# Kernel tuning notes

Measured on AMD Instinct MI355X. Metric: run time of the kernel, lower is better.

The kernel has to match this reference:

```python
import jax, jax.numpy as jnp
import numpy as np

DEG = [1, 72, 201, 816, 1790, 3756, 6923, 12768, 20286, 31710, 51623, 82296, 124280, 177576, 251115, 326064, 395760, 456840, 506179, 516200, 507003, 493746, 489256, 453936, 420025, 411320, 427761, 420700, 420500, 426780, 414284, 407008, 394053, 360910, 322245, 313704, 282902, 270940, 237783, 209000, 193766, 177870, 162110, 144848, 121230, 112700, 93483, 88512, 72275, 80700, 68799, 56784, 42665, 30996, 25630, 12936, 9804, 8584, 5251, 3480, 3111, 2728, 1890, 1472, 1235, 330, 201, 68, 69, 0, 71]
_d = np.array(DEG, dtype=np.float64)
AVG_LOG = float((np.log(np.arange(len(_d)) + 1.0) * _d).sum() / _d.sum())  # avg_deg['log']

N_NODES, N_EDGES, N_GRAPHS = 10000, 100000, 64
TOWERS, F, F_OUT, N_LAYERS = 5, 75, 15, 4


def setup_inputs() -> dict:
    key = jax.random.key(0)
    ks = jax.random.split(key, 32)
    r = lambda i, shape: jax.random.normal(ks[i], shape, jnp.float32) * 0.1
    return {
        "x": jax.random.normal(ks[0], (N_NODES, 14), jnp.float32),
        "edge_index": jax.random.randint(ks[1], (2, N_EDGES), 0, N_NODES, dtype=jnp.int32),
        "edge_attr": jax.random.normal(ks[2], (N_EDGES, 4), jnp.float32),
        "batch": jnp.sort(jax.random.randint(ks[3], (N_NODES,), 0, N_GRAPHS, dtype=jnp.int32)),
        "node_emb_w": r(4, (14, F)), "node_emb_b": r(5, (F,)),
        "edge_emb_w": r(6, (4, 50)), "edge_emb_b": r(7, (50,)),
        "ee_w": r(8, (N_LAYERS, 50, F)), "ee_b": r(9, (N_LAYERS, F)),
        "pre_w": r(10, (N_LAYERS, TOWERS, 3 * F, F)), "pre_b": r(11, (N_LAYERS, TOWERS, F)),
        "post_w": r(12, (N_LAYERS, TOWERS, 13 * F, F_OUT)), "post_b": r(13, (N_LAYERS, TOWERS, F_OUT)),
        "lin_w": r(14, (N_LAYERS, F, F)), "lin_b": r(15, (N_LAYERS, F)),
        "bn_g": jnp.ones((N_LAYERS, F), jnp.float32), "bn_b": jnp.zeros((N_LAYERS, F), jnp.float32),
        "mlp_w1": r(16, (F, 50)), "mlp_b1": r(17, (50,)),
        "mlp_w2": r(18, (50, 25)), "mlp_b2": r(19, (25,)),
        "mlp_w3": r(20, (25, 1)), "mlp_b3": r(21, (1,)),
    }


def _pna_conv(x, src, dst, ea, ee_w, ee_b, pre_w, pre_b, post_w, post_b, lin_w, lin_b):
    # x: [N, F]; ea: [E, edge_dim]; divide_input=False so every tower sees full F.
    N = x.shape[0]
    e = ea @ ee_w + ee_b                                   # edge_encoder  [E, F]
    h = jnp.concatenate([x[dst], x[src], e], axis=-1)       # [x_i, x_j, e] [E, 3F]
    m = jnp.einsum('ef,tfg->etg', h, pre_w) + pre_b         # per-tower pre nn [E, T, F]
    cnt = jax.ops.segment_sum(jnp.ones((m.shape[0],), x.dtype), dst, N)  # in-degree [N]
    cnt1 = jnp.maximum(cnt, 1.0)[:, None, None]
    mean = jax.ops.segment_sum(m, dst, N) / cnt1
    mean_sq = jax.ops.segment_sum(m * m, dst, N) / cnt1
    std = jnp.sqrt(jax.nn.relu(mean_sq - mean * mean) + 1e-5)
    has = (cnt > 0)[:, None, None]
    mn = jnp.where(has, jax.ops.segment_min(m, dst, N), 0.0)
    mx = jnp.where(has, jax.ops.segment_max(m, dst, N), 0.0)
    agg = jnp.concatenate([mean, mn, mx, std], axis=-1)     # [N, T, 4F]
    scl = jnp.log(cnt1 + 1.0) / AVG_LOG                     # amplification scaler
    out = jnp.concatenate([agg, agg * scl, agg / scl], -1)  # identity/amp/atten [N, T, 12F]
    x_rep = jnp.broadcast_to(x[:, None, :], (N, TOWERS, x.shape[1]))
    out = jnp.concatenate([x_rep, out], axis=-1)            # [N, T, 13F]
    out = jnp.einsum('ntf,tfg->ntg', out, post_w) + post_b  # per-tower post nn [N, T, F_out]
    return out.reshape(N, -1) @ lin_w + lin_b               # [N, F]


def _bn(x, g, b):
    mu = x.mean(0)
    var = x.var(0)  # biased, as torch BatchNorm1d uses for normalization
    return (x - mu) * jax.lax.rsqrt(var + 1e-5) * g + b


def reference(x, edge_index, edge_attr, batch, node_emb_w, node_emb_b, edge_emb_w, edge_emb_b,
              ee_w, ee_b, pre_w, pre_b, post_w, post_b, lin_w, lin_b, bn_g, bn_b,
              mlp_w1, mlp_b1, mlp_w2, mlp_b2, mlp_w3, mlp_b3):
    src, dst = edge_index[0], edge_index[1]
    h = x @ node_emb_w + node_emb_b
    ea = edge_attr @ edge_emb_w + edge_emb_b
    for i in range(N_LAYERS):
        h = jax.nn.relu(_bn(_pna_conv(h, src, dst, ea, ee_w[i], ee_b[i], pre_w[i], pre_b[i],
                                      post_w[i], post_b[i], lin_w[i], lin_b[i]), bn_g[i], bn_b[i]))
    per_atom = h
    g = jax.ops.segment_sum(h, batch, N_GRAPHS)             # global_add_pool [G, F]
    g = jax.nn.relu(g @ mlp_w1 + mlp_b1)
    g = jax.nn.relu(g @ mlp_w2 + mlp_b2)
    g = (g @ mlp_w3 + mlp_b3).reshape(-1)                   # num_out==1 -> view(-1)
    return (g, per_atom)
```

## Files before the change

### kernel.cpp

```cpp
#include <hip/hip_runtime.h>
#include <math.h>

#define NN 10000
#define NE 100000
#define NGR 64
#define NT 5
#define FD 75
#define FOUT 15
#define NLAY 4
#define MAXB 1792

typedef __bf16 bf16;
typedef __bf16 bf16x8 __attribute__((ext_vector_type(8)));
typedef float f32x4 __attribute__((ext_vector_type(4)));

__device__ inline unsigned pk2(float a, float b) {
  bf16 x = (bf16)a, y = (bf16)b;
  unsigned short ux, uy;
  __builtin_memcpy(&ux, &x, 2); __builtin_memcpy(&uy, &y, 2);
  return (unsigned)ux | ((unsigned)uy << 16);
}


__global__ __launch_bounds__(256) void k_node_emb(const float* __restrict__ x,
    const float* __restrict__ w, const float* __restrict__ b, bf16* __restrict__ hbf) {
  int idx = blockIdx.x * 256 + threadIdx.x;
  if (idx >= NN * FD) return;
  int n = idx / FD, f = idx - n * FD;
  float acc = b[f];
#pragma unroll
  for (int k = 0; k < 14; ++k) acc += x[n * 14 + k] * w[k * FD + f];
  hbf[n * 80 + f] = (bf16)acc;
}

__global__ __launch_bounds__(256) void k_hpad(bf16* __restrict__ hbf) {
  int idx = blockIdx.x * 256 + threadIdx.x;
  if (idx >= NN * 5) return;
  int n = idx / 5, f = 75 + idx % 5;
  hbf[n * 80 + f] = (bf16)0.f;
}

__global__ __launch_bounds__(256) void k_edge4(const float* __restrict__ eattr,
    bf16* __restrict__ eabf4) {
  int idx = blockIdx.x * 256 + threadIdx.x;
  if (idx >= NE * 8) return;
  int e = idx >> 3, c = idx & 7;
  eabf4[idx] = (c < 4) ? (bf16)eattr[e * 4 + c] : (bf16)0.f;
}

__global__ __launch_bounds__(256) void k_count(const int* __restrict__ dst, int* __restrict__ deg) {
  int e = blockIdx.x * 256 + threadIdx.x;
  if (e < NE) atomicAdd(&deg[dst[e]], 1);
}

__global__ __launch_bounds__(1024) void k_scan(const int* __restrict__ deg, int* __restrict__ rowptr) {
  __shared__ int buf[1024];
  __shared__ int carry;
  int tid = threadIdx.x;
  if (tid == 0) carry = 0;
  __syncthreads();
  for (int base = 0; base < NN; base += 1024) {
    int i = base + tid;
    int v = (i < NN) ? deg[i] : 0;
    buf[tid] = v;
    __syncthreads();
    for (int off = 1; off < 1024; off <<= 1) {
      int t = (tid >= off) ? buf[tid - off] : 0;
      __syncthreads();
      buf[tid] += t;
      __syncthreads();
    }
    int inc = buf[tid];
    int tot = buf[1023];
    if (i < NN) rowptr[i + 1] = carry + inc;
    __syncthreads();
    if (tid == 0) carry += tot;
    __syncthreads();
  }
  if (tid == 0) rowptr[0] = 0;
}

__global__ __launch_bounds__(256) void k_scl(const int* __restrict__ deg, float* __restrict__ scl,
                                             float* __restrict__ iscl, float inv_avg_log) {
  int n = blockIdx.x * 256 + threadIdx.x;
  if (n >= NN) return;
  float c1 = fmaxf((float)deg[n], 1.f);
  float s = logf(c1 + 1.f) * inv_avg_log;
  scl[n] = s;
  iscl[n] = 1.f / s;
}

__global__ __launch_bounds__(256) void k_scatter(const int* __restrict__ dst, const int* __restrict__ rowptr,
    int* __restrict__ cursor, int* __restrict__ eids) {
  int e = blockIdx.x * 256 + threadIdx.x;
  if (e >= NE) return;
  int d = dst[e];
  int pos = rowptr[d] + atomicAdd(&cursor[d], 1);
  eids[pos] = e;
}

__global__ __launch_bounds__(256) void k_next(const int* __restrict__ rowptr, int* __restrict__ nxt) {
  int n = blockIdx.x * 256 + threadIdx.x;
  if (n >= NN) return;
  int base = rowptr[n];
  int lo = n + 1, hi = min(n + 128, NN);
  while (lo < hi) {
    int mid = (lo + hi + 1) >> 1;
    if (rowptr[mid] - base <= 128) lo = mid; else hi = mid - 1;
  }
  nxt[n] = lo;
}

__global__ __launch_bounds__(1024) void k_walk(const int* __restrict__ nxt,
    int* __restrict__ bstart, int* __restrict__ nblk) {
  __shared__ int lnx[NN];
  int tid = threadIdx.x;
  for (int i = tid; i < NN; i += 1024) lnx[i] = nxt[i];
  __syncthreads();
  if (tid == 0) {
    int b = 0, n = 0;
    while (n < NN && b < MAXB) { bstart[b++] = n; n = lnx[n]; }
    bstart[b] = NN;
    nblk[0] = b;
  }
}


__global__ __launch_bounds__(256) void k_W12(const float* __restrict__ ew,
    const float* __restrict__ ebias, const float* __restrict__ ee_wA, const float* __restrict__ ee_bA,
    float* __restrict__ W12A, float* __restrict__ bcombA) {
  const int l = blockIdx.y;
  const float* ee_w = ee_wA + (size_t)l * 50 * FD;
  const float* ee_b = ee_bA + (size_t)l * FD;
  int idx = blockIdx.x * 256 + threadIdx.x;
  if (idx >= 375) return;
  if (idx < 300) {
    int d = idx / 75, o = idx - d * 75;
    float v = 0.f;
    for (int j = 0; j < 50; ++j) v += ew[d * 50 + j] * ee_w[j * 75 + o];
    W12A[(size_t)l * 300 + idx] = v;
  } else {
    int o = idx - 300;
    float v = ee_b[o];
    for (int j = 0; j < 50; ++j) v += ebias[j] * ee_w[j * 75 + o];
    bcombA[(size_t)l * 80 + o] = v;
  }
}

__global__ __launch_bounds__(256) void k_combine(const float* __restrict__ pre_wA,
    const float* __restrict__ pre_bA, const float* __restrict__ W12A, const float* __restrict__ bcombA,
    bf16* __restrict__ WctA, float* __restrict__ bcA) {
  const int l = blockIdx.y;
  const float* pre_w = pre_wA + (size_t)l * NT * 225 * FD;
  const float* pre_b = pre_bA + (size_t)l * NT * FD;
  const float* W12   = W12A + (size_t)l * 300;
  const float* bcomb = bcombA + (size_t)l * 80;
  bf16* Wct = WctA + (size_t)l * 384 * 192;
  float* bc = bcA + (size_t)l * 384;
  int idx = blockIdx.x * 256 + threadIdx.x;
  if (idx >= 384 * 192) return;
  int c = idx / 192, s = idx - c * 192;
  int t = c / 75, g = c - t * 75;
  int chunk = s >> 6, within = s & 63, sblk = within >> 3, elem = within & 7;
  int lb = sblk ^ (c & 7);
  int k = chunk * 64 + lb * 8 + elem;
  float v = 0.f;
  if (c < 375) {
    if (k < 75)                    v = pre_w[(t * 225 + k) * 75 + g];
    else if (k >= 80 && k < 155)   v = pre_w[(t * 225 + 75 + (k - 80)) * 75 + g];
    else if (k >= 160 && k < 164) {
      int d = k - 160;
      float a = 0.f;
      for (int f2 = 0; f2 < 75; ++f2) a += W12[d * 75 + f2] * pre_w[(t * 225 + 150 + f2) * 75 + g];
      v = a;
    }
  }
  Wct[c * 192 + s] = (bf16)v;
  if (s == 0) {
    float a = 0.f;
    if (c < 375) {
      a = pre_b[t * 75 + g];
      for (int f2 = 0; f2 < 75; ++f2) a += bcomb[f2] * pre_w[(t * 225 + 150 + f2) * 75 + g];
    }
    bc[c] = a;
  }
}

__global__ __launch_bounds__(256) void k_PL(const float* __restrict__ pwA,
    const float* __restrict__ lwA, float* __restrict__ PLA) {
  const int l = blockIdx.y;
  const float* pw = pwA + (size_t)l * NT * 975 * FOUT;
  const float* lw = lwA + (size_t)l * FD * FD;
  float* PL = PLA + (size_t)l * 5 * 975 * 80;
  int idx = blockIdx.x * 256 + threadIdx.x;
  if (idx >= 5 * 975 * 80) return;
  int t = idx / (975 * 80), rem = idx - t * 975 * 80;
  int row = rem / 80, o = rem - row * 80;
  float v = 0.f;
  if (o < 75) {
#pragma unroll
    for (int j = 0; j < 15; ++j)
      v += pw[((size_t)t * 975 + row) * 15 + j] * lw[(t * 15 + j) * 75 + o];
  }
  PL[idx] = v;
}

__global__ __launch_bounds__(256) void k_combine2b(const float* __restrict__ PLA,
    bf16* __restrict__ Wct2A) {
  const int l = blockIdx.y;
  const float* PL = PLA + (size_t)l * 5 * 975 * 80;
  bf16* Wct2 = Wct2A + (size_t)l * 256 * 1664;
  int idx = blockIdx.x * 256 + threadIdx.x;
  if (idx >= 256 * 1664) return;
  int c = idx / 1664, s = idx - c * 1664;
  int chunk = s >> 6, within = s & 63, sblk = within >> 3, elem = within & 7;
  int lb = sblk ^ (c & 7);
  int k = chunk * 64 + lb * 8 + elem;
  int g2 = c / 80, o = c - g2 * 80;
  float val = 0.f;
  if (c < 240 && o < 75) {
    if (k < 75) {
      if (g2 == 0) {
#pragma unroll
        for (int t = 0; t < 5; ++t) val += PL[(t * 975 + k) * 80 + o];
      }
    } else if (k >= 80 && k < 1616) {
      int q = k - 80;
      int si = q / 384, cc = q - si * 384;
      if (cc < 375) {
        int t = cc / 75, g = cc - t * 75;
        int row = 75 + g2 * 300 + si * 75 + g;
        val = PL[((size_t)t * 975 + row) * 80 + o];
      }
    }
  }
  Wct2[(size_t)c * 1664 + s] = (bf16)val;
}

__global__ __launch_bounds__(128) void k_zbias(const float* __restrict__ pbA,
    const float* __restrict__ lwA, const float* __restrict__ lbA, float* __restrict__ zbA) {
  const int l = blockIdx.y;
  const float* pb = pbA + (size_t)l * NT * FOUT;
  const float* lw = lwA + (size_t)l * FD * FD;
  const float* lb = lbA + (size_t)l * FD;
  float* zb = zbA + (size_t)l * 80;
  int o = threadIdx.x;
  if (o >= 80) return;
  float val = 0.f;
  if (o < 75) {
    val = lb[o];
    for (int t = 0; t < 5; ++t)
      for (int j = 0; j < 15; ++j)
        val += pb[t * 15 + j] * lw[(t * 15 + j) * 75 + o];
  }
  zb[o] = val;
}


#define LOADB(ntb_, c_) do {                                                      \
    const bf16* wp_ = Wct + (size_t)((ntb_) + sr) * 192 + (c_) * 64 + slb * 8;    \
    pq0 = *(const uint4*)(wp_ + 0 * 6144);                                        \
    pq1 = *(const uint4*)(wp_ + 1 * 6144);                                        \
    pq2 = *(const uint4*)(wp_ + 2 * 6144);                                        \
    pq3 = *(const uint4*)(wp_ + 3 * 6144); } while (0)

#define STOREB(BS_) do {                                          \
    *(uint4*)((BS_) + (0 * 32 + sr) * 128 + (slb << 4)) = pq0;    \
    *(uint4*)((BS_) + (1 * 32 + sr) * 128 + (slb << 4)) = pq1;    \
    *(uint4*)((BS_) + (2 * 32 + sr) * 128 + (slb << 4)) = pq2;    \
    *(uint4*)((BS_) + (3 * 32 + sr) * 128 + (slb << 4)) = pq3; } while (0)

#define DO_KK(BS_, KB_, A0_, A1_, A2_, A3_) do {                         \
    bf16x8 af0 = *(const bf16x8*)(A0_);                                  \
    bf16x8 af1 = *(const bf16x8*)(A1_);                                  \
    bf16x8 af2 = *(const bf16x8*)(A2_);                                  \
    bf16x8 af3 = *(const bf16x8*)(A3_);                                  \
    const unsigned char* bp_ = (BS_) + (((KB_) ^ (l15 & 7)) << 4) + wc * 8192 + l15 * 128; \
    bf16x8 bv0 = *(const bf16x8*)(bp_ + 0 * 2048);                       \
    bf16x8 bv1 = *(const bf16x8*)(bp_ + 1 * 2048);                       \
    bf16x8 bv2 = *(const bf16x8*)(bp_ + 2 * 2048);                       \
    bf16x8 bv3 = *(const bf16x8*)(bp_ + 3 * 2048);                       \
    acc[0][0] = __builtin_amdgcn_mfma_f32_16x16x32_bf16(af0, bv0, acc[0][0], 0, 0, 0); \
    acc[1][0] = __builtin_amdgcn_mfma_f32_16x16x32_bf16(af1, bv0, acc[1][0], 0, 0, 0); \
    acc[2][0] = __builtin_amdgcn_mfma_f32_16x16x32_bf16(af2, bv0, acc[2][0], 0, 0, 0); \
    acc[3][0] = __builtin_amdgcn_mfma_f32_16x16x32_bf16(af3, bv0, acc[3][0], 0, 0, 0); \
    acc[0][1] = __builtin_amdgcn_mfma_f32_16x16x32_bf16(af0, bv1, acc[0][1], 0, 0, 0); \
    acc[1][1] = __builtin_amdgcn_mfma_f32_16x16x32_bf16(af1, bv1, acc[1][1], 0, 0, 0); \
    acc[2][1] = __builtin_amdgcn_mfma_f32_16x16x32_bf16(af2, bv1, acc[2][1], 0, 0, 0); \
    acc[3][1] = __builtin_amdgcn_mfma_f32_16x16x32_bf16(af3, bv1, acc[3][1], 0, 0, 0); \
    acc[0][2] = __builtin_amdgcn_mfma_f32_16x16x32_bf16(af0, bv2, acc[0][2], 0, 0, 0); \
    acc[1][2] = __builtin_amdgcn_mfma_f32_16x16x32_bf16(af1, bv2, acc[1][2], 0, 0, 0); \
    acc[2][2] = __builtin_amdgcn_mfma_f32_16x16x32_bf16(af2, bv2, acc[2][2], 0, 0, 0); \
    acc[3][2] = __builtin_amdgcn_mfma_f32_16x16x32_bf16(af3, bv2, acc[3][2], 0, 0, 0); \
    acc[0][3] = __builtin_amdgcn_mfma_f32_16x16x32_bf16(af0, bv3, acc[0][3], 0, 0, 0); \
    acc[1][3] = __builtin_amdgcn_mfma_f32_16x16x32_bf16(af1, bv3, acc[1][3], 0, 0, 0); \
    acc[2][3] = __builtin_amdgcn_mfma_f32_16x16x32_bf16(af2, bv3, acc[2][3], 0, 0, 0); \
    acc[3][3] = __builtin_amdgcn_mfma_f32_16x16x32_bf16(af3, bv3, acc[3][3], 0, 0, 0); \
  } while (0)

__global__ __launch_bounds__(256) void k_pre_fused(
    const bf16* __restrict__ hbf, const int* __restrict__ eids,
    const int* __restrict__ srcA, const int* __restrict__ dstA,
    const int* __restrict__ rowptr, const int* __restrict__ bstart, const int* __restrict__ nblk,
    const bf16* __restrict__ Wct, const float* __restrict__ bc,
    bf16* __restrict__ aggbf2, unsigned eoff_base) {
  __shared__ __align__(16) unsigned char smem[33792];
  unsigned char* Bs0 = smem;
  unsigned char* Bs1 = smem + 16384;
  bf16* m_lds = (bf16*)smem;
  __shared__ unsigned dOffL[128], sOffL[128], eOffL[128];
  __shared__ int nodeRows[129];
  __shared__ int nq[5];

  const int b = blockIdx.x;
  if (b >= nblk[0]) return;
  const int ntb = blockIdx.y * 128;
  const int tid = threadIdx.x;
  const int n0b = bstart[b], n1b = bstart[b + 1];
  const int rbase = rowptr[n0b];
  const int nrows = rowptr[n1b] - rbase;
  const int nnod = n1b - n0b;

  if (tid == 0) { nq[0] = 0; nq[1] = 0; nq[2] = 0; nq[3] = 0; nq[4] = nnod; }
  if (tid < 128) {
    int e = (tid < nrows) ? eids[rbase + tid] : 0;
    dOffL[tid] = (unsigned)(dstA[e] * 160);
    sOffL[tid] = (unsigned)(srcA[e] * 160);
    eOffL[tid] = eoff_base + (unsigned)(e * 16);
  }
  if (tid <= nnod) nodeRows[tid] = rowptr[n0b + tid] - rbase;
  __syncthreads();
  if (tid < nnod) {
#pragma unroll
    for (int q = 1; q <= 3; ++q) {
      int target = (nrows * q) >> 2;
      if (nodeRows[tid] < target && nodeRows[tid + 1] >= target) nq[q] = tid + 1;
    }
  }

  const int lane = tid & 63;
  const int wave = tid >> 6;
  const int wr = wave >> 1, wc = wave & 1;
  const int l15 = lane & 15, l4 = lane >> 4;
  const int sr = tid >> 3, slb = tid & 7;

  const unsigned char* hb = (const unsigned char*)hbf;
  const int ar = wr * 64 + l15;
  const unsigned dof0 = dOffL[ar], dof1 = dOffL[ar + 16], dof2 = dOffL[ar + 32], dof3 = dOffL[ar + 48];
  const unsigned sof0 = sOffL[ar], sof1 = sOffL[ar + 16], sof2 = sOffL[ar + 32], sof3 = sOffL[ar + 48];
  const unsigned eof0 = eOffL[ar], eof1 = eOffL[ar + 16], eof2 = eOffL[ar + 32], eof3 = eOffL[ar + 48];

  f32x4 acc[4][4];
  f32x4 zv = {0.f, 0.f, 0.f, 0.f};
#pragma unroll
  for (int i = 0; i < 4; ++i)
#pragma unroll
    for (int j = 0; j < 4; ++j) acc[i][j] = zv;

  uint4 pq0, pq1, pq2, pq3;
  LOADB(ntb, 0);

  STOREB(Bs0);
  __syncthreads();
  LOADB(ntb, 1);
  DO_KK(Bs0, l4,     hb + dof0 + l4 * 16, hb + dof1 + l4 * 16, hb + dof2 + l4 * 16, hb + dof3 + l4 * 16);
  DO_KK(Bs0, 4 + l4, hb + dof0 + 64 + l4 * 16, hb + dof1 + 64 + l4 * 16, hb + dof2 + 64 + l4 * 16, hb + dof3 + 64 + l4 * 16);

  STOREB(Bs1);
  __syncthreads();
  LOADB(ntb, 2);
  {
    unsigned o0 = (l4 < 2) ? (dof0 + 128 + l4 * 16) : (sof0 + (l4 - 2) * 16);
    unsigned o1 = (l4 < 2) ? (dof1 + 128 + l4 * 16) : (sof1 + (l4 - 2) * 16);
    unsigned o2 = (l4 < 2) ? (dof2 + 128 + l4 * 16) : (sof2 + (l4 - 2) * 16);
    unsigned o3 = (l4 < 2) ? (dof3 + 128 + l4 * 16) : (sof3 + (l4 - 2) * 16);
    DO_KK(Bs1, l4, hb + o0, hb + o1, hb + o2, hb + o3);
  }
  DO_KK(Bs1, 4 + l4, hb + sof0 + 32 + l4 * 16, hb + sof1 + 32 + l4 * 16, hb + sof2 + 32 + l4 * 16, hb + sof3 + 32 + l4 * 16);

  STOREB(Bs0);
  __syncthreads();
  DO_KK(Bs0, l4, hb + sof0 + 96 + l4 * 16, hb + sof1 + 96 + l4 * 16, hb + sof2 + 96 + l4 * 16, hb + sof3 + 96 + l4 * 16);
  DO_KK(Bs0, 4 + l4, hb + eof0 + l4 * 16, hb + eof1 + l4 * 16, hb + eof2 + l4 * 16, hb + eof3 + l4 * 16);
  __syncthreads();

  float bcv[4];
#pragma unroll
  for (int j = 0; j < 4; ++j) bcv[j] = bc[ntb + wc * 64 + j * 16 + l15];
#pragma unroll
  for (int i = 0; i < 4; ++i) {
    int R = wr * 64 + i * 16 + l4 * 4;
#pragma unroll
    for (int j = 0; j < 4; ++j) {
      int col = wc * 64 + j * 16 + l15;
#pragma unroll
      for (int q = 0; q < 4; ++q)
        m_lds[(R + q) * 132 + col] = (bf16)(acc[i][j][q] + bcv[j]);
    }
  }
  __syncthreads();

  {
    const int cp = tid & 63;
    const int qq = tid >> 6;
    const unsigned char* mb = (const unsigned char*)m_lds;
    for (int i = nq[qq]; i < nq[qq + 1]; ++i) {
      int ra = nodeRows[i], rb2 = nodeRows[i + 1];
      float s0 = 0.f, q0 = 0.f, a0 = INFINITY, b0 = -INFINITY;
      float s1 = 0.f, q1 = 0.f, a1 = INFINITY, b1 = -INFINITY;
      for (int r = ra; r < rb2; ++r) {
        unsigned u = *(const unsigned*)(mb + r * 264 + cp * 4);
        float v0 = __uint_as_float(u << 16);
        float v1 = __uint_as_float(u & 0xffff0000u);
        s0 += v0; q0 += v0 * v0; a0 = fminf(a0, v0); b0 = fmaxf(b0, v0);
        s1 += v1; q1 += v1 * v1; a1 = fminf(a1, v1); b1 = fmaxf(b1, v1);
      }
      int d = rb2 - ra;
      float inv = 1.f / ((d > 0) ? (float)d : 1.f);
      float m0 = s0 * inv, m1 = s1 * inv;
      float sd0 = sqrtf(fmaxf(q0 * inv - m0 * m0, 0.f) + 1e-5f);
      float sd1 = sqrtf(fmaxf(q1 * inv - m1 * m1, 0.f) + 1e-5f);
      if (d == 0) { a0 = 0.f; b0 = 0.f; a1 = 0.f; b1 = 0.f; }
      bf16* ag = aggbf2 + (size_t)(n0b + i) * 1536 + ntb + cp * 2;
      *(unsigned*)(ag)        = pk2(m0, m1);
      *(unsigned*)(ag + 384)  = pk2(a0, a1);
      *(unsigned*)(ag + 768)  = pk2(b0, b1);
      *(unsigned*)(ag + 1152) = pk2(sd0, sd1);
    }
  }
}


#define APG_(g_) ((nA >= NN || (g_) >= 202) ? zerobuf : \
    ((g_) < 10 ? hbf + nA * 80 + (g_) * 8 : aggbf2 + (size_t)nA * 1536 + ((g_) - 10) * 8))

#define LOADP4(c_) do {                                                 \
    int gA_ = (c_) * 16 + slb;                                          \
    pa0 = *(const uint4*)APG_(gA_);                                     \
    pa1 = *(const uint4*)APG_(gA_ + 8);                                 \
    int ko_ = (c_) * 128 + slb * 8;                                     \
    pb0 = *(const uint4*)(pc0 + ko_);                                   \
    pb1 = *(const uint4*)(pc0 + ko_ + 64);                              \
    pb2 = *(const uint4*)(pc1 + ko_);                                   \
    pb3 = *(const uint4*)(pc1 + ko_ + 64);                              \
    pb4 = *(const uint4*)(pc2 + ko_);                                   \
    pb5 = *(const uint4*)(pc2 + ko_ + 64);                              \
    pb6 = *(const uint4*)(pc3 + ko_);                                   \
    pb7 = *(const uint4*)(pc3 + ko_ + 64);                              \
  } while (0)

__global__ __launch_bounds__(256) void k_post4(const bf16* __restrict__ hbf,
    const bf16* __restrict__ aggbf2, const bf16* __restrict__ Wct2,
    const float* __restrict__ zb, const float* __restrict__ scl, const float* __restrict__ iscl,
    const bf16* __restrict__ zerobuf, float* __restrict__ z, float* __restrict__ stat_raw_l) {
  __shared__ __align__(16) unsigned char smem[40960];
  unsigned char* As = smem;
  unsigned char* Bs = smem + 8192;
  float* Ps = (float*)smem;
  __shared__ float sclS[32], isclS[32];
  const int n0 = blockIdx.x * 32;
  const int y  = blockIdx.y;
  const int tid = threadIdx.x;
  const int lane = tid & 63, wave = tid >> 6;
  const int l15 = lane & 15, l4 = lane >> 4;
  const int sr = tid >> 3, slb = tid & 7;
  const int nA = n0 + sr;

  const bf16 *pc0, *pc1, *pc2, *pc3;
  {
    int c0 = sr, c1 = sr + 32, c2 = sr + 64, c3 = sr + 96;
    int l0 = (c0 / 40) * 80 + y * 40 + (c0 % 40);
    int l1 = (c1 / 40) * 80 + y * 40 + (c1 % 40);
    int l2 = (c2 / 40) * 80 + y * 40 + (c2 % 40);
    int l3 = (c3 < 120) ? ((c3 / 40) * 80 + y * 40 + (c3 % 40)) : 0;
    pc0 = Wct2 + (size_t)l0 * 1664;
    pc1 = Wct2 + (size_t)l1 * 1664;
    pc2 = Wct2 + (size_t)l2 * 1664;
    pc3 = Wct2 + (size_t)l3 * 1664;
  }
  if (tid < 32) {
    int n = n0 + tid;
    sclS[tid] = (n < NN) ? scl[n] : 0.f;
    isclS[tid] = (n < NN) ? iscl[n] : 0.f;
  }

  f32x4 acc[2][2];
  f32x4 zvv = {0.f, 0.f, 0.f, 0.f};
#pragma unroll
  for (int i = 0; i < 2; ++i)
#pragma unroll
    for (int j = 0; j < 2; ++j) acc[i][j] = zvv;

  uint4 pa0, pa1, pb0, pb1, pb2, pb3, pb4, pb5, pb6, pb7;
  LOADP4(0);
  for (int c = 0; c < 13; ++c) {
    {
      int s1_ = (slb ^ (sr & 7)) << 4;
      *(uint4*)(As + sr * 256 + s1_) = pa0;
      *(uint4*)(As + sr * 256 + s1_ + 128) = pa1;
      *(uint4*)(Bs + (sr)      * 256 + (slb << 4)) = pb0;
      *(uint4*)(Bs + (sr)      * 256 + (slb << 4) + 128) = pb1;
      *(uint4*)(Bs + (sr + 32) * 256 + (slb << 4)) = pb2;
      *(uint4*)(Bs + (sr + 32) * 256 + (slb << 4) + 128) = pb3;
      *(uint4*)(Bs + (sr + 64) * 256 + (slb << 4)) = pb4;
      *(uint4*)(Bs + (sr + 64) * 256 + (slb << 4) + 128) = pb5;
      *(uint4*)(Bs + (sr + 96) * 256 + (slb << 4)) = pb6;
      *(uint4*)(Bs + (sr + 96) * 256 + (slb << 4) + 128) = pb7;
    }
    __syncthreads();
    if (c < 12) LOADP4(c + 1);
#pragma unroll
    for (int kk = 0; kk < 4; ++kk) {
      int kb = kk * 4 + l4;
      bf16x8 af[2], bv[2];
#pragma unroll
      for (int i = 0; i < 2; ++i) {
        int row = i * 16 + l15;
        af[i] = *(const bf16x8*)(As + row * 256 + (((kb & 8) | ((kb & 7) ^ (row & 7))) << 4));
      }
#pragma unroll
      for (int j = 0; j < 2; ++j) {
        int cidx = wave * 32 + j * 16 + l15;
        bv[j] = *(const bf16x8*)(Bs + cidx * 256 + (((kb & 8) | ((kb & 7) ^ (cidx & 7))) << 4));
      }
#pragma unroll
      for (int i = 0; i < 2; ++i)
#pragma unroll
        for (int j = 0; j < 2; ++j)
          acc[i][j] = __builtin_amdgcn_mfma_f32_16x16x32_bf16(af[i], bv[j], acc[i][j], 0, 0, 0);
    }
    __syncthreads();
  }

#pragma unroll
  for (int i = 0; i < 2; ++i) {
#pragma unroll
    for (int j = 0; j < 2; ++j) {
      int cidx = wave * 32 + j * 16 + l15;
#pragma unroll
      for (int q = 0; q < 4; ++q)
        Ps[(i * 16 + l4 * 4 + q) * 132 + cidx] = acc[i][j][q];
    }
  }
  __syncthreads();

  float v0_, v1_, v2_, v3_, v4_;
  int r0_, r1_, r2_, r3_, r4_, f0_, f1_, f2_, f3_, f4_;
#define EPI(t_, vv_, rr_, ff_) do {                                           \
    int idx_ = tid + (t_) * 256;                                              \
    rr_ = idx_ / 40; ff_ = idx_ - rr_ * 40;                                   \
    int n_ = n0 + rr_, zc_ = y * 40 + ff_;                                    \
    float v_ = 0.f;                                                           \
    if (n_ < NN && zc_ < 75) {                                                \
      v_ = Ps[rr_ * 132 + ff_] + sclS[rr_] * Ps[rr_ * 132 + 40 + ff_]         \
         + isclS[rr_] * Ps[rr_ * 132 + 80 + ff_] + zb[zc_];                   \
      z[n_ * 75 + zc_] = v_;                                                  \
    }                                                                         \
    vv_ = v_;                                                                 \
  } while (0)
  EPI(0, v0_, r0_, f0_); EPI(1, v1_, r1_, f1_); EPI(2, v2_, r2_, f2_);
  EPI(3, v3_, r3_, f3_); EPI(4, v4_, r4_, f4_);
#undef EPI
  __syncthreads();
  Ps[r0_ * 132 + f0_] = v0_;
  Ps[r1_ * 132 + f1_] = v1_;
  Ps[r2_ * 132 + f2_] = v2_;
  Ps[r3_ * 132 + f3_] = v3_;
  Ps[r4_ * 132 + f4_] = v4_;
  __syncthreads();
  if (tid < 40) {
    int zc = y * 40 + tid;
    if (zc < 75) {
      float s = 0.f, s2 = 0.f;
#pragma unroll
      for (int r = 0; r < 32; ++r) {
        float v = Ps[r * 132 + tid];
        s += v; s2 += v * v;
      }
      atomicAdd(&stat_raw_l[zc], s);
      atomicAdd(&stat_raw_l[75 + zc], s2);
    }
  }
}

__global__ __launch_bounds__(256) void k_bnapply(const float* __restrict__ z,
    const float* __restrict__ stat_raw, const float* __restrict__ g, const float* __restrict__ b,
    float* __restrict__ outF, bf16* __restrict__ hbf,
    const int* __restrict__ batch, float* __restrict__ gpool) {
  int idx = blockIdx.x * 256 + threadIdx.x;
  if (idx >= NN * FD) return;
  int n = idx / FD, f = idx - n * FD;
  float mu = stat_raw[f] * (1.f / NN);
  float var = stat_raw[75 + f] * (1.f / NN) - mu * mu;
  var = fmaxf(var, 0.f);
  float rs = 1.f / sqrtf(var + 1e-5f);
  float v = (z[idx] - mu) * rs * g[f] + b[f];
  v = fmaxf(v, 0.f);
  if (outF) {
    outF[idx] = v;
    atomicAdd(&gpool[batch[n] * FD + f], v);
  }
  hbf[n * 80 + f] = (bf16)v;
}

__global__ __launch_bounds__(128) void k_mlp2(const float* __restrict__ gpool,
    const float* __restrict__ w1, const float* __restrict__ b1,
    const float* __restrict__ w2, const float* __restrict__ b2,
    const float* __restrict__ w3, const float* __restrict__ b3,
    float* __restrict__ out) {
  __shared__ float G[75];
  __shared__ float H1[50];
  __shared__ float H2[25];
  const int gr = blockIdx.x;
  const int tid = threadIdx.x;
  if (tid < 75) G[tid] = gpool[gr * FD + tid];
  __syncthreads();
  if (tid < 50) {
    float a = b1[tid];
    for (int k = 0; k < 75; ++k) a += G[k] * w1[k * 50 + tid];
    H1[tid] = fmaxf(a, 0.f);
  }
  __syncthreads();
  if (tid < 25) {
    float a = b2[tid];
    for (int k = 0; k < 50; ++k) a += H1[k] * w2[k * 25 + tid];
    H2[tid] = fmaxf(a, 0.f);
  }
  __syncthreads();
  if (tid == 0) {
    float a = b3[0];
    for (int k = 0; k < 25; ++k) a += H2[k] * w3[k];
    out[gr] = a;
  }
}


extern "C" void kernel_launch(void* const* d_in, const int* in_sizes, int n_in,
                              void* d_out, int out_size, void* d_ws, size_t ws_size,
                              hipStream_t stream) {
  (void)in_sizes; (void)n_in; (void)out_size; (void)ws_size;
  const float* x      = (const float*)d_in[0];
  const int*   eidx   = (const int*)  d_in[1];
  const float* eattr  = (const float*)d_in[2];
  const int*   batch  = (const int*)  d_in[3];
  const float* nw     = (const float*)d_in[4];
  const float* nb     = (const float*)d_in[5];
  const float* ew     = (const float*)d_in[6];
  const float* ebias  = (const float*)d_in[7];
  const float* ee_w   = (const float*)d_in[8];
  const float* ee_b   = (const float*)d_in[9];
  const float* pre_w  = (const float*)d_in[10];
  const float* pre_b  = (const float*)d_in[11];
  const float* post_w = (const float*)d_in[12];
  const float* post_b = (const float*)d_in[13];
  const float* lin_w  = (const float*)d_in[14];
  const float* lin_b  = (const float*)d_in[15];
  const float* bn_g   = (const float*)d_in[16];
  const float* bn_b   = (const float*)d_in[17];
  const float* w1 = (const float*)d_in[18];
  const float* b1 = (const float*)d_in[19];
  const float* w2 = (const float*)d_in[20];
  const float* b2 = (const float*)d_in[21];
  const float* w3 = (const float*)d_in[22];
  const float* b3 = (const float*)d_in[23];

  const int* srcA = eidx;
  const int* dstA = eidx + NE;

  char* base = (char*)d_ws;
  size_t off = 0;
  auto alloc = [&](size_t bytes) -> char* {
    char* p = base + off;
    off = (off + bytes + 255) & ~(size_t)255;
    return p;
  };
  bf16*  hbf    = (bf16*) alloc((size_t)NN * 80 * 2);
  bf16*  eabf4  = (bf16*) alloc((size_t)NE * 8 * 2 + 64);
  bf16*  aggbf2 = (bf16*) alloc((size_t)NN * 1536 * 2);
  float* z      = (float*)alloc((size_t)NN * FD * 4);
  bf16*  WctA   = (bf16*) alloc((size_t)NLAY * 384 * 192 * 2);
  float* bcA    = (float*)alloc((size_t)NLAY * 384 * 4);
  bf16*  Wct2A  = (bf16*) alloc((size_t)NLAY * 256 * 1664 * 2);
  float* zbA    = (float*)alloc((size_t)NLAY * 80 * 4);
  float* PLA    = (float*)alloc((size_t)NLAY * 5 * 975 * 80 * 4);
  float* W12A   = (float*)alloc((size_t)NLAY * 300 * 4);
  float* bcombA = (float*)alloc((size_t)NLAY * 80 * 4);
  float* scl    = (float*)alloc(NN * 4);
  float* iscl   = (float*)alloc(NN * 4);
  int*   deg    = (int*)alloc(NN * 4);
  int*   rowptr = (int*)alloc((NN + 1) * 4);
  int*   cursor = (int*)alloc(NN * 4);
  int*   eids   = (int*)alloc(NE * 4);
  int*   nxt    = (int*)alloc(NN * 4);
  int*   bstart = (int*)alloc((MAXB + 1) * 4);
  int*   nblk   = (int*)alloc(16);
  float* stat_all = (float*)alloc((size_t)NLAY * 160 * 4);
  float* gpool  = (float*)alloc(NGR * FD * 4);
  bf16*  zerobuf = (bf16*)alloc(256);

  const unsigned eoff_base = (unsigned)((char*)eabf4 - (char*)hbf);

  static const int DEG_TAB[71] = {1, 72, 201, 816, 1790, 3756, 6923, 12768, 20286, 31710,
    51623, 82296, 124280, 177576, 251115, 326064, 395760, 456840, 506179, 516200, 507003,
    493746, 489256, 453936, 420025, 411320, 427761, 420700, 420500, 426780, 414284, 407008,
    394053, 360910, 322245, 313704, 282902, 270940, 237783, 209000, 193766, 177870, 162110,
    144848, 121230, 112700, 93483, 88512, 72275, 80700, 68799, 56784, 42665, 30996, 25630,
    12936, 9804, 8584, 5251, 3480, 3111, 2728, 1890, 1472, 1235, 330, 201, 68, 69, 0, 71};
  double num = 0.0, den = 0.0;
  for (int i = 0; i < 71; ++i) { num += log((double)i + 1.0) * DEG_TAB[i]; den += DEG_TAB[i]; }
  float inv_avg_log = (float)(den / num);

  hipMemsetAsync(deg, 0, NN * 4, stream);
  hipMemsetAsync(cursor, 0, NN * 4, stream);
  hipMemsetAsync(gpool, 0, NGR * FD * 4, stream);
  hipMemsetAsync(stat_all, 0, (size_t)NLAY * 160 * 4, stream);
  hipMemsetAsync(zerobuf, 0, 256, stream);

  k_node_emb<<<(NN * FD + 255) / 256, 256, 0, stream>>>(x, nw, nb, hbf);
  k_hpad<<<(NN * 5 + 255) / 256, 256, 0, stream>>>(hbf);
  k_edge4<<<(NE * 8 + 255) / 256, 256, 0, stream>>>(eattr, eabf4);
  k_count<<<(NE + 255) / 256, 256, 0, stream>>>(dstA, deg);
  k_scan<<<1, 1024, 0, stream>>>(deg, rowptr);
  k_scl<<<(NN + 255) / 256, 256, 0, stream>>>(deg, scl, iscl, inv_avg_log);
  k_scatter<<<(NE + 255) / 256, 256, 0, stream>>>(dstA, rowptr, cursor, eids);
  k_next<<<(NN + 255) / 256, 256, 0, stream>>>(rowptr, nxt);
  k_walk<<<1, 1024, 0, stream>>>(nxt, bstart, nblk);

  {
    dim3 gw(2, NLAY);
    k_W12<<<gw, 256, 0, stream>>>(ew, ebias, ee_w, ee_b, W12A, bcombA);
    dim3 gc((384 * 192 + 255) / 256, NLAY);
    k_combine<<<gc, 256, 0, stream>>>(pre_w, pre_b, W12A, bcombA, WctA, bcA);
    dim3 gp((5 * 975 * 80 + 255) / 256, NLAY);
    k_PL<<<gp, 256, 0, stream>>>(post_w, lin_w, PLA);
    dim3 g2((256 * 1664 + 255) / 256, NLAY);
    k_combine2b<<<g2, 256, 0, stream>>>(PLA, Wct2A);
    dim3 gz(1, NLAY);
    k_zbias<<<gz, 128, 0, stream>>>(post_b, lin_w, lin_b, zbA);
  }

  float* outp = (float*)d_out;
  for (int l = 0; l < NLAY; ++l) {
    dim3 gpref(MAXB, 3);
    k_pre_fused<<<gpref, 256, 0, stream>>>(hbf, eids, srcA, dstA, rowptr, bstart, nblk,
        WctA + (size_t)l * 384 * 192, bcA + (size_t)l * 384, aggbf2, eoff_base);
    dim3 gpost((NN + 31) / 32, 2);
    k_post4<<<gpost, 256, 0, stream>>>(hbf, aggbf2, Wct2A + (size_t)l * 256 * 1664,
        zbA + (size_t)l * 80, scl, iscl, zerobuf, z, stat_all + (size_t)l * 160);
    float* wdst = (l == NLAY - 1) ? (outp + NGR) : nullptr;
    k_bnapply<<<(NN * FD + 255) / 256, 256, 0, stream>>>(z, stat_all + (size_t)l * 160,
        bn_g + (size_t)l * FD, bn_b + (size_t)l * FD, wdst, hbf, batch, gpool);
  }

  k_mlp2<<<NGR, 128, 0, stream>>>(gpool, w1, b1, w2, b2, w3, b3, outp);
}
```

Before: 493.6 us.

## Double post-GEMM node tile and read A fragments directly from global memory

The post-aggregation GEMM kernel now covers 64 nodes per block instead of 32, so each block reuses the staged weight tile across twice as many rows and fewer weight bytes are loaded per node. The A operand (node features plus aggregates) is no longer staged through shared memory. Each lane loads its MFMA fragments straight from global memory, with bounds and segment selection done per load. This removes A shared-memory stores and some traffic, but the direct global loads inside the MFMA loop are not prefetched, so their latency may be exposed. The grid also shrinks to about 157x2 blocks, which reduces parallelism.

Result: slower. 590.0 us (+19.5%).

```diff
diff --git a/kernel.cpp b/kernel.cpp
--- a/kernel.cpp
+++ b/kernel.cpp
@@ -431,13 +431,7 @@
 }
 
 
-#define APG_(g_) ((nA >= NN || (g_) >= 202) ? zerobuf : \
-    ((g_) < 10 ? hbf + nA * 80 + (g_) * 8 : aggbf2 + (size_t)nA * 1536 + ((g_) - 10) * 8))
-
-#define LOADP4(c_) do {                                                 \
-    int gA_ = (c_) * 16 + slb;                                          \
-    pa0 = *(const uint4*)APG_(gA_);                                     \
-    pa1 = *(const uint4*)APG_(gA_ + 8);                                 \
+#define LOADPB(c_) do {                                                 \
     int ko_ = (c_) * 128 + slb * 8;                                     \
     pb0 = *(const uint4*)(pc0 + ko_);                                   \
     pb1 = *(const uint4*)(pc0 + ko_ + 64);                              \
@@ -449,22 +443,23 @@
     pb7 = *(const uint4*)(pc3 + ko_ + 64);                              \
   } while (0)
 
+#define PAPTR(hb_, ab_, ok_, off_) ((ok_) ? ((off_) < 80 ? (hb_) + (off_) : \
+    ((off_) < 1616 ? (ab_) + (off_) : zerobuf)) : zerobuf)
+
 __global__ __launch_bounds__(256) void k_post4(const bf16* __restrict__ hbf,
     const bf16* __restrict__ aggbf2, const bf16* __restrict__ Wct2,
     const float* __restrict__ zb, const float* __restrict__ scl, const float* __restrict__ iscl,
     const bf16* __restrict__ zerobuf, float* __restrict__ z, float* __restrict__ stat_raw_l) {
-  __shared__ __align__(16) unsigned char smem[40960];
-  unsigned char* As = smem;
-  unsigned char* Bs = smem + 8192;
+  __shared__ __align__(16) unsigned char smem[33792];
+  unsigned char* Bs = smem;
   float* Ps = (float*)smem;
-  __shared__ float sclS[32], isclS[32];
-  const int n0 = blockIdx.x * 32;
+  __shared__ float sclS[64], isclS[64];
+  const int n0 = blockIdx.x * 64;
   const int y  = blockIdx.y;
   const int tid = threadIdx.x;
   const int lane = tid & 63, wave = tid >> 6;
   const int l15 = lane & 15, l4 = lane >> 4;
   const int sr = tid >> 3, slb = tid & 7;
-  const int nA = n0 + sr;
 
   const bf16 *pc0, *pc1, *pc2, *pc3;
   {
@@ -478,62 +473,73 @@
     pc2 = Wct2 + (size_t)l2 * 1664;
     pc3 = Wct2 + (size_t)l3 * 1664;
   }
-  if (tid < 32) {
+  if (tid < 64) {
     int n = n0 + tid;
     sclS[tid] = (n < NN) ? scl[n] : 0.f;
     isclS[tid] = (n < NN) ? iscl[n] : 0.f;
   }
 
-  f32x4 acc[2][2];
+  const int na0 = n0 + 0 * 16 + l15, na1 = n0 + 1 * 16 + l15;
+  const int na2 = n0 + 2 * 16 + l15, na3 = n0 + 3 * 16 + l15;
+  const bool ok0 = na0 < NN, ok1 = na1 < NN, ok2 = na2 < NN, ok3 = na3 < NN;
+  const bf16* hb0 = hbf + na0 * 80;
+  const bf16* hb1 = hbf + na1 * 80;
+  const bf16* hb2 = hbf + na2 * 80;
+  const bf16* hb3 = hbf + na3 * 80;
+  const bf16* ab0 = aggbf2 + (size_t)na0 * 1536 - 80;
+  const bf16* ab1 = aggbf2 + (size_t)na1 * 1536 - 80;
+  const bf16* ab2 = aggbf2 + (size_t)na2 * 1536 - 80;
+  const bf16* ab3 = aggbf2 + (size_t)na3 * 1536 - 80;
+
+  f32x4 acc[4][2];
   f32x4 zvv = {0.f, 0.f, 0.f, 0.f};
 #pragma unroll
-  for (int i = 0; i < 2; ++i)
+  for (int i = 0; i < 4; ++i)
 #pragma unroll
     for (int j = 0; j < 2; ++j) acc[i][j] = zvv;
 
-  uint4 pa0, pa1, pb0, pb1, pb2, pb3, pb4, pb5, pb6, pb7;
-  LOADP4(0);
+  uint4 pb0, pb1, pb2, pb3, pb4, pb5, pb6, pb7;
+  LOADPB(0);
   for (int c = 0; c < 13; ++c) {
-    {
-      int s1_ = (slb ^ (sr & 7)) << 4;
-      *(uint4*)(As + sr * 256 + s1_) = pa0;
-      *(uint4*)(As + sr * 256 + s1_ + 128) = pa1;
-      *(uint4*)(Bs + (sr)      * 256 + (slb << 4)) = pb0;
-      *(uint4*)(Bs + (sr)      * 256 + (slb << 4) + 128) = pb1;
-      *(uint4*)(Bs + (sr + 32) * 256 + (slb << 4)) = pb2;
-      *(uint4*)(Bs + (sr + 32) * 256 + (slb << 4) + 128) = pb3;
-      *(uint4*)(Bs + (sr + 64) * 256 + (slb << 4)) = pb4;
-      *(uint4*)(Bs + (sr + 64) * 256 + (slb << 4) + 128) = pb5;
-      *(uint4*)(Bs + (sr + 96) * 256 + (slb << 4)) = pb6;
-      *(uint4*)(Bs + (sr + 96) * 256 + (slb << 4) + 128) = pb7;
-    }
+    *(uint4*)(Bs + (sr)      * 256 + (slb << 4)) = pb0;
+    *(uint4*)(Bs + (sr)      * 256 + (slb << 4) + 128) = pb1;
+    *(uint4*)(Bs + (sr + 32) * 256 + (slb << 4)) = pb2;
+    *(uint4*)(Bs + (sr + 32) * 256 + (slb << 4) + 128) = pb3;
+    *(uint4*)(Bs + (sr + 64) * 256 + (slb << 4)) = pb4;
+    *(uint4*)(Bs + (sr + 64) * 256 + (slb << 4) + 128) = pb5;
+    *(uint4*)(Bs + (sr + 96) * 256 + (slb << 4)) = pb6;
+    *(uint4*)(Bs + (sr + 96) * 256 + (slb << 4) + 128) = pb7;
     __syncthreads();
-    if (c < 12) LOADP4(c + 1);
+    if (c < 12) LOADPB(c + 1);
 #pragma unroll
     for (int kk = 0; kk < 4; ++kk) {
       int kb = kk * 4 + l4;
-      bf16x8 af[2], bv[2];
-#pragma unroll
-      for (int i = 0; i < 2; ++i) {
-        int row = i * 16 + l15;
-        af[i] = *(const bf16x8*)(As + row * 256 + (((kb & 8) | ((kb & 7) ^ (row & 7))) << 4));
+      int off = c * 128 + kb * 8;
+      bf16x8 af0 = *(const bf16x8*)PAPTR(hb0, ab0, ok0, off);
+      bf16x8 af1 = *(const bf16x8*)PAPTR(hb1, ab1, ok1, off);
+      bf16x8 af2 = *(const bf16x8*)PAPTR(hb2, ab2, ok2, off);
+      bf16x8 af3 = *(const bf16x8*)PAPTR(hb3, ab3, ok3, off);
+      bf16x8 bv0, bv1;
+      {
+        int cidx0 = wave * 32 + l15;
+        int cidx1 = wave * 32 + 16 + l15;
+        bv0 = *(const bf16x8*)(Bs + cidx0 * 256 + (((kb & 8) | ((kb & 7) ^ (cidx0 & 7))) << 4));
+        bv1 = *(const bf16x8*)(Bs + cidx1 * 256 + (((kb & 8) | ((kb & 7) ^ (cidx1 & 7))) << 4));
       }
-#pragma unroll
-      for (int j = 0; j < 2; ++j) {
-        int cidx = wave * 32 + j * 16 + l15;
-        bv[j] = *(const bf16x8*)(Bs + cidx * 256 + (((kb & 8) | ((kb & 7) ^ (cidx & 7))) << 4));
-      }
-#pragma unroll
-      for (int i = 0; i < 2; ++i)
-#pragma unroll
-        for (int j = 0; j < 2; ++j)
-          acc[i][j] = __builtin_amdgcn_mfma_f32_16x16x32_bf16(af[i], bv[j], acc[i][j], 0, 0, 0);
+      acc[0][0] = __builtin_amdgcn_mfma_f32_16x16x32_bf16(af0, bv0, acc[0][0], 0, 0, 0);
+      acc[1][0] = __builtin_amdgcn_mfma_f32_16x16x32_bf16(af1, bv0, acc[1][0], 0, 0, 0);
+      acc[2][0] = __builtin_amdgcn_mfma_f32_16x16x32_bf16(af2, bv0, acc[2][0], 0, 0, 0);
+      acc[3][0] = __builtin_amdgcn_mfma_f32_16x16x32_bf16(af3, bv0, acc[3][0], 0, 0, 0);
+      acc[0][1] = __builtin_amdgcn_mfma_f32_16x16x32_bf16(af0, bv1, acc[0][1], 0, 0, 0);
+      acc[1][1] = __builtin_amdgcn_mfma_f32_16x16x32_bf16(af1, bv1, acc[1][1], 0, 0, 0);
+      acc[2][1] = __builtin_amdgcn_mfma_f32_16x16x32_bf16(af2, bv1, acc[2][1], 0, 0, 0);
+      acc[3][1] = __builtin_amdgcn_mfma_f32_16x16x32_bf16(af3, bv1, acc[3][1], 0, 0, 0);
     }
     __syncthreads();
   }
 
 #pragma unroll
-  for (int i = 0; i < 2; ++i) {
+  for (int i = 0; i < 4; ++i) {
 #pragma unroll
     for (int j = 0; j < 2; ++j) {
       int cidx = wave * 32 + j * 16 + l15;
@@ -544,36 +550,32 @@
   }
   __syncthreads();
 
-  float v0_, v1_, v2_, v3_, v4_;
-  int r0_, r1_, r2_, r3_, r4_, f0_, f1_, f2_, f3_, f4_;
-#define EPI(t_, vv_, rr_, ff_) do {                                           \
-    int idx_ = tid + (t_) * 256;                                              \
-    rr_ = idx_ / 40; ff_ = idx_ - rr_ * 40;                                   \
-    int n_ = n0 + rr_, zc_ = y * 40 + ff_;                                    \
-    float v_ = 0.f;                                                           \
-    if (n_ < NN && zc_ < 75) {                                                \
-      v_ = Ps[rr_ * 132 + ff_] + sclS[rr_] * Ps[rr_ * 132 + 40 + ff_]         \
-         + isclS[rr_] * Ps[rr_ * 132 + 80 + ff_] + zb[zc_];                   \
-      z[n_ * 75 + zc_] = v_;                                                  \
-    }                                                                         \
-    vv_ = v_;                                                                 \
-  } while (0)
-  EPI(0, v0_, r0_, f0_); EPI(1, v1_, r1_, f1_); EPI(2, v2_, r2_, f2_);
-  EPI(3, v3_, r3_, f3_); EPI(4, v4_, r4_, f4_);
-#undef EPI
-  __syncthreads();
-  Ps[r0_ * 132 + f0_] = v0_;
-  Ps[r1_ * 132 + f1_] = v1_;
-  Ps[r2_ * 132 + f2_] = v2_;
-  Ps[r3_ * 132 + f3_] = v3_;
-  Ps[r4_ * 132 + f4_] = v4_;
+  float vv[10];
+  int rrA[10], ffA[10];
+#pragma unroll
+  for (int t = 0; t < 10; ++t) {
+    int idx = tid + t * 256;
+    int rr = idx / 40, ff = idx - rr * 40;
+    rrA[t] = rr; ffA[t] = ff;
+    int n_ = n0 + rr, zc = y * 40 + ff;
+    float v = 0.f;
+    if (n_ < NN && zc < 75) {
+      v = Ps[rr * 132 + ff] + sclS[rr] * Ps[rr * 132 + 40 + ff]
+        + isclS[rr] * Ps[rr * 132 + 80 + ff] + zb[zc];
+      z[n_ * 75 + zc] = v;
+    }
+    vv[t] = v;
+  }
+  __syncthreads();
+#pragma unroll
+  for (int t = 0; t < 10; ++t) Ps[rrA[t] * 132 + ffA[t]] = vv[t];
   __syncthreads();
   if (tid < 40) {
     int zc = y * 40 + tid;
     if (zc < 75) {
       float s = 0.f, s2 = 0.f;
 #pragma unroll
-      for (int r = 0; r < 32; ++r) {
+      for (int r = 0; r < 64; ++r) {
         float v = Ps[r * 132 + tid];
         s += v; s2 += v * v;
       }
@@ -744,7 +746,7 @@
     dim3 gpref(MAXB, 3);
     k_pre_fused<<<gpref, 256, 0, stream>>>(hbf, eids, srcA, dstA, rowptr, bstart, nblk,
         WctA + (size_t)l * 384 * 192, bcA + (size_t)l * 384, aggbf2, eoff_base);
-    dim3 gpost((NN + 31) / 32, 2);
+    dim3 gpost((NN + 63) / 64, 2);
     k_post4<<<gpost, 256, 0, stream>>>(hbf, aggbf2, Wct2A + (size_t)l * 256 * 1664,
         zbA + (size_t)l * 80, scl, iscl, zerobuf, z, stat_all + (size_t)l * 160);
     float* wdst = (l == NLAY - 1) ? (outp + NGR) : nullptr;
```
